# Kernel optimization log

Hardware: AMD Instinct MI355X
Metric: run time of the kernel (lower is better)

## Reference

```python
import jax, jax.numpy as jnp
import numpy as np

D_DIM = 128
K_DIM = 32


def setup_inputs() -> dict:
    key = jax.random.key(0)
    k1, k2, k3 = jax.random.split(key, 3)
    B, H, W = 8, 64, 64
    std1 = 1.0 / (K_DIM * D_DIM) ** 0.5
    std2 = 1.0 / K_DIM ** 0.5
    X = jax.random.normal(k1, (B, D_DIM, H, W), dtype=jnp.float32)
    codewords = jax.random.uniform(k2, (K_DIM, D_DIM), dtype=jnp.float32, minval=-std1, maxval=std1)
    scale = jax.random.uniform(k3, (K_DIM,), dtype=jnp.float32, minval=-std2, maxval=std2)
    return {"X": X, "codewords": codewords, "scale": scale}


def reference(X, codewords, scale):
    # X: [B, D, H, W] -> descriptors [B, N, D]
    B, D, H, W = X.shape
    Xf = X.reshape(B, D, H * W).transpose(0, 2, 1)  # [B, N, D]
    # Squared distance ||x - c||^2 expanded: avoids materializing [B,N,K,D]
    x_sq = jnp.sum(Xf * Xf, axis=-1, keepdims=True)          # [B, N, 1]
    c_sq = jnp.sum(codewords * codewords, axis=-1)           # [K]
    cross = jnp.einsum('bnd,kd->bnk', Xf, codewords)         # [B, N, K]
    dist2 = x_sq - 2.0 * cross + c_sq                        # [B, N, K]
    # NOTE: faithful to source -- softmax over scale * dist^2 (no negation)
    A = jax.nn.softmax(dist2 * scale, axis=-1)               # [B, N, K]
    # E[b,k,d] = sum_n A[b,n,k] * (x[b,n,d] - c[k,d])
    E = jnp.einsum('bnk,bnd->bkd', A, Xf) - jnp.sum(A, axis=1)[..., None] * codewords
    return E  # [B, K, D]
```

## Files before the change

kernel.cpp:

```cpp
#include <hip/hip_runtime.h>
#include <hip/hip_bf16.h>

#define D_DIM 128
#define K_DIM 32
#define NPIX  4096
#define TPB   128

typedef __bf16 bf16x8 __attribute__((ext_vector_type(8)));
typedef unsigned short u16x8 __attribute__((ext_vector_type(8)));
typedef float f32x4 __attribute__((ext_vector_type(4)));

__device__ __forceinline__ unsigned short f2bf(float f) {
    union { float f; unsigned u; } v; v.f = f;
    unsigned r = v.u + 0x7FFFu + ((v.u >> 16) & 1u);
    return (unsigned short)(r >> 16);
}
__device__ __forceinline__ unsigned pack2(float lo, float hi) {
    __hip_bfloat162 h = __float22bfloat162_rn(make_float2(lo, hi));
    union { __hip_bfloat162 b; unsigned u; } u; u.b = h;
    return u.u;
}
__device__ __forceinline__ float bf2f(unsigned short u) {
    union { unsigned u; float f; } v; v.u = ((unsigned)u) << 16;
    return v.f;
}
__device__ __forceinline__ bf16x8 ldfrag(const unsigned short* p) {
    union { u16x8 s; bf16x8 b; } u;
    u.s = *(const u16x8*)p;
    return u.b;
}
__device__ __forceinline__ bf16x8 pack8(float4 a, float4 b) {
    union { unsigned d[4]; bf16x8 v; } u;
    u.d[0] = pack2(a.x, a.y); u.d[1] = pack2(a.z, a.w);
    u.d[2] = pack2(b.x, b.y); u.d[3] = pack2(b.z, b.w);
    return u.v;
}

#define XND_LD 136
#define CW_LD  136
#define SA_LD  136

__global__ __launch_bounds__(256, 2) void enc_kernel(
    const float* __restrict__ X,
    const float* __restrict__ cw,
    const float* __restrict__ scale,
    float* __restrict__ out)
{
    __shared__ __align__(16) unsigned short sXnd[TPB * XND_LD];
    __shared__ __align__(16) unsigned short sCW[K_DIM * CW_LD];
    __shared__ __align__(16) unsigned short sA[K_DIM * SA_LD];
    __shared__ float sXsqP[8 * 129];
    __shared__ float sXsq[TPB];
    __shared__ float sSum[K_DIM];
    __shared__ float sSc[K_DIM];
    __shared__ float sCS[K_DIM];

    const int ltid = threadIdx.x;
    const int b    = blockIdx.x >> 5;
    const int n0   = (blockIdx.x & 31) * TPB;
    const int lane = ltid & 63;
    const int w    = ltid >> 6;
    const int l15  = lane & 15;
    const int quad = lane >> 4;

    if (ltid < K_DIM) {
        const float4* cr = (const float4*)(cw + ltid * D_DIM);
        float cs = 0.f;
        #pragma unroll 8
        for (int q = 0; q < 32; ++q) {
            float4 c4 = cr[q];
            cs = fmaf(c4.x, c4.x, fmaf(c4.y, c4.y, fmaf(c4.z, c4.z, fmaf(c4.w, c4.w, cs))));
        }
        float s = scale[ltid];
        sSc[ltid] = s;
        sCS[ltid] = cs * s;
        sSum[ltid] = 0.f;
    }

    {
        const int r  = ltid >> 3;
        const int q8 = ltid & 7;
        const float* cr = cw + r * D_DIM + 16 * q8;
        float4 c0 = *(const float4*)(cr + 0);
        float4 c1 = *(const float4*)(cr + 4);
        float4 c2 = *(const float4*)(cr + 8);
        float4 c3 = *(const float4*)(cr + 12);
        uint4 p0, p1;
        p0.x = pack2(c0.x, c0.y); p0.y = pack2(c0.z, c0.w);
        p0.z = pack2(c1.x, c1.y); p0.w = pack2(c1.z, c1.w);
        p1.x = pack2(c2.x, c2.y); p1.y = pack2(c2.z, c2.w);
        p1.z = pack2(c3.x, c3.y); p1.w = pack2(c3.z, c3.w);
        *(uint4*)&sCW[r * CW_LD + 16 * q8 + 0] = p0;
        *(uint4*)&sCW[r * CW_LD + 16 * q8 + 8] = p1;
    }

    {
        const int c = ltid & 31;
        const int r = ltid >> 5;
        float px[4] = {0.f, 0.f, 0.f, 0.f};
        const float* xb = X + (size_t)b * D_DIM * NPIX + n0;
        #pragma unroll
        for (int p = 0; p < 8; ++p) {
            const int d0 = 2 * (r + 8 * p);
            float4 f0 = *(const float4*)(xb + (size_t)d0 * NPIX + 4 * c);
            float4 f1 = *(const float4*)(xb + (size_t)(d0 + 1) * NPIX + 4 * c);
            px[0] = fmaf(f0.x, f0.x, fmaf(f1.x, f1.x, px[0]));
            px[1] = fmaf(f0.y, f0.y, fmaf(f1.y, f1.y, px[1]));
            px[2] = fmaf(f0.z, f0.z, fmaf(f1.z, f1.z, px[2]));
            px[3] = fmaf(f0.w, f0.w, fmaf(f1.w, f1.w, px[3]));
            *(unsigned*)&sXnd[(4 * c + 0) * XND_LD + d0] = pack2(f0.x, f1.x);
            *(unsigned*)&sXnd[(4 * c + 1) * XND_LD + d0] = pack2(f0.y, f1.y);
            *(unsigned*)&sXnd[(4 * c + 2) * XND_LD + d0] = pack2(f0.z, f1.z);
            *(unsigned*)&sXnd[(4 * c + 3) * XND_LD + d0] = pack2(f0.w, f1.w);
        }
        #pragma unroll
        for (int j = 0; j < 4; ++j) sXsqP[r * 129 + 4 * c + j] = px[j];
    }
    __syncthreads();

    if (ltid < TPB) {
        float s = 0.f;
        #pragma unroll
        for (int r = 0; r < 8; ++r) s += sXsqP[r * 129 + ltid];
        sXsq[ltid] = s;
    }

    f32x4 accA[2][2] = {{{0.f,0.f,0.f,0.f},{0.f,0.f,0.f,0.f}},
                        {{0.f,0.f,0.f,0.f},{0.f,0.f,0.f,0.f}}};
    {
        const int prow0 = (32 * w + l15) * XND_LD;
        const int prow1 = (32 * w + 16 + l15) * XND_LD;
        #pragma unroll
        for (int ks = 0; ks < 4; ++ks) {
            const int off = 8 * quad + 32 * ks;
            bf16x8 a0 = ldfrag(&sCW[l15 * CW_LD + off]);
            bf16x8 a1 = ldfrag(&sCW[(l15 + 16) * CW_LD + off]);
            bf16x8 b0 = ldfrag(&sXnd[prow0 + off]);
            bf16x8 b1 = ldfrag(&sXnd[prow1 + off]);
            accA[0][0] = __builtin_amdgcn_mfma_f32_16x16x32_bf16(a0, b0, accA[0][0], 0, 0, 0);
            accA[0][1] = __builtin_amdgcn_mfma_f32_16x16x32_bf16(a1, b0, accA[0][1], 0, 0, 0);
            accA[1][0] = __builtin_amdgcn_mfma_f32_16x16x32_bf16(a0, b1, accA[1][0], 0, 0, 0);
            accA[1][1] = __builtin_amdgcn_mfma_f32_16x16x32_bf16(a1, b1, accA[1][1], 0, 0, 0);
        }
    }
    __syncthreads();

    {
        float r8[8] = {0.f,0.f,0.f,0.f,0.f,0.f,0.f,0.f};
        #pragma unroll
        for (int pt = 0; pt < 2; ++pt) {
            const float xsq = sXsq[32 * w + 16 * pt + l15];
            float e8[8];
            float psum = 0.f;
            #pragma unroll
            for (int mt = 0; mt < 2; ++mt)
                #pragma unroll
                for (int reg = 0; reg < 4; ++reg) {
                    const int k = 16 * mt + 4 * quad + reg;
                    float l = fmaf(sSc[k], fmaf(-2.f, accA[pt][mt][reg], xsq), sCS[k]);
                    float e = __expf(l);
                    e8[4 * mt + reg] = e;
                    psum += e;
                }
            psum += __shfl_xor(psum, 16);
            psum += __shfl_xor(psum, 32);
            const float inv = 1.f / psum;
            #pragma unroll
            for (int i = 0; i < 8; ++i) {
                e8[i] *= inv;
                r8[i] += e8[i];
            }
            #pragma unroll
            for (int mt = 0; mt < 2; ++mt)
                #pragma unroll
                for (int reg = 0; reg < 4; ++reg) {
                    const int k = 16 * mt + 4 * quad + reg;
                    sA[k * SA_LD + 32 * w + 16 * pt + l15] = f2bf(e8[4 * mt + reg]);
                }
        }
        #pragma unroll
        for (int i = 0; i < 8; ++i) {
            r8[i] += __shfl_xor(r8[i], 1);
            r8[i] += __shfl_xor(r8[i], 2);
            r8[i] += __shfl_xor(r8[i], 4);
            r8[i] += __shfl_xor(r8[i], 8);
        }
        if (l15 == 0) {
            #pragma unroll
            for (int mt = 0; mt < 2; ++mt)
                #pragma unroll
                for (int reg = 0; reg < 4; ++reg)
                    atomicAdd(&sSum[16 * mt + 4 * quad + reg], r8[4 * mt + reg]);
        }
    }
    __syncthreads();

    f32x4 accE[2][2] = {{{0.f,0.f,0.f,0.f},{0.f,0.f,0.f,0.f}},
                        {{0.f,0.f,0.f,0.f},{0.f,0.f,0.f,0.f}}};
    #pragma unroll
    for (int dt = 0; dt < 2; ++dt) {
        const int d = 16 * (2 * w + dt) + l15;
        const float* xrow = X + ((size_t)b * D_DIM + d) * NPIX + n0;
        float4 g[4][2];
        #pragma unroll
        for (int ks = 0; ks < 4; ++ks) {
            const float* p = xrow + 8 * quad + 32 * ks;
            g[ks][0] = *(const float4*)p;
            g[ks][1] = *(const float4*)(p + 4);
        }
        #pragma unroll
        for (int ks = 0; ks < 4; ++ks) {
            const int off = 8 * quad + 32 * ks;
            bf16x8 bfrag = pack8(g[ks][0], g[ks][1]);
            bf16x8 a0 = ldfrag(&sA[l15 * SA_LD + off]);
            bf16x8 a1 = ldfrag(&sA[(l15 + 16) * SA_LD + off]);
            accE[dt][0] = __builtin_amdgcn_mfma_f32_16x16x32_bf16(a0, bfrag, accE[dt][0], 0, 0, 0);
            accE[dt][1] = __builtin_amdgcn_mfma_f32_16x16x32_bf16(a1, bfrag, accE[dt][1], 0, 0, 0);
        }
    }

    {
        float* outb = out + (size_t)b * (K_DIM * D_DIM);
        #pragma unroll
        for (int dt = 0; dt < 2; ++dt) {
            const int d = 16 * (2 * w + dt) + l15;
            #pragma unroll
            for (int mt = 0; mt < 2; ++mt) {
                #pragma unroll
                for (int rr = 0; rr < 4; ++rr) {
                    const int reg = (rr + blockIdx.x) & 3;
                    const int k = 16 * mt + 4 * quad + reg;
                    float sk  = sSum[k];
                    float cwv = bf2f(sCW[k * CW_LD + d]);
                    float v = fmaf(-sk, cwv, accE[dt][mt][reg]);
                    atomicAdd(outb + k * D_DIM + d, v);
                }
            }
        }
    }
}

extern "C" void kernel_launch(void* const* d_in, const int* in_sizes, int n_in,
                              void* d_out, int out_size, void* d_ws, size_t ws_size,
                              hipStream_t stream) {
    const float* X  = (const float*)d_in[0];
    const float* cw = (const float*)d_in[1];
    const float* sc = (const float*)d_in[2];
    float* out = (float*)d_out;
    (void)in_sizes; (void)n_in; (void)d_ws; (void)ws_size; (void)out_size;

    hipLaunchKernelGGL(enc_kernel, dim3(256), dim3(256), 0, stream, X, cw, sc, out);
}
```

Before: 71.82 us.

## Swizzle X tile in LDS with 16-byte stores and drop xsq reduction barrier

Restructures the X staging so each thread loads 8 consecutive channels and writes one packed 16-byte chunk per pixel into an XOR-swizzled LDS layout, replacing many 4-byte scattered stores. The MFMA B-fragment reads apply the matching swizzle. It also removes the separate x-squared reduction pass and its __syncthreads: each lane now sums the partial norms itself right before the softmax. The goal is fewer LDS bank conflicts and store instructions plus one less barrier, at the cost of some redundant LDS reads for the norm sums and more live registers.

```diff
diff --git a/kernel.cpp b/kernel.cpp
--- a/kernel.cpp
+++ b/kernel.cpp
@@ -50,7 +50,6 @@
     __shared__ __align__(16) unsigned short sCW[K_DIM * CW_LD];
     __shared__ __align__(16) unsigned short sA[K_DIM * SA_LD];
     __shared__ float sXsqP[8 * 129];
-    __shared__ float sXsq[TPB];
     __shared__ float sSum[K_DIM];
     __shared__ float sSc[K_DIM];
     __shared__ float sCS[K_DIM];
@@ -100,56 +99,73 @@
         float px[4] = {0.f, 0.f, 0.f, 0.f};
         const float* xb = X + (size_t)b * D_DIM * NPIX + n0;
         #pragma unroll
-        for (int p = 0; p < 8; ++p) {
-            const int d0 = 2 * (r + 8 * p);
-            float4 f0 = *(const float4*)(xb + (size_t)d0 * NPIX + 4 * c);
-            float4 f1 = *(const float4*)(xb + (size_t)(d0 + 1) * NPIX + 4 * c);
-            px[0] = fmaf(f0.x, f0.x, fmaf(f1.x, f1.x, px[0]));
-            px[1] = fmaf(f0.y, f0.y, fmaf(f1.y, f1.y, px[1]));
-            px[2] = fmaf(f0.z, f0.z, fmaf(f1.z, f1.z, px[2]));
-            px[3] = fmaf(f0.w, f0.w, fmaf(f1.w, f1.w, px[3]));
-            *(unsigned*)&sXnd[(4 * c + 0) * XND_LD + d0] = pack2(f0.x, f1.x);
-            *(unsigned*)&sXnd[(4 * c + 1) * XND_LD + d0] = pack2(f0.y, f1.y);
-            *(unsigned*)&sXnd[(4 * c + 2) * XND_LD + d0] = pack2(f0.z, f1.z);
-            *(unsigned*)&sXnd[(4 * c + 3) * XND_LD + d0] = pack2(f0.w, f1.w);
+        for (int h = 0; h < 2; ++h) {
+            float fx[8], fy[8], fz[8], fw[8];
+            #pragma unroll
+            for (int dd = 0; dd < 8; ++dd) {
+                const int d = 64 * h + 8 * r + dd;
+                float4 f = *(const float4*)(xb + (size_t)d * NPIX + 4 * c);
+                fx[dd] = f.x; fy[dd] = f.y; fz[dd] = f.z; fw[dd] = f.w;
+                px[0] = fmaf(f.x, f.x, px[0]);
+                px[1] = fmaf(f.y, f.y, px[1]);
+                px[2] = fmaf(f.z, f.z, px[2]);
+                px[3] = fmaf(f.w, f.w, px[3]);
+            }
+            const int pchunk = (r ^ (c & 7)) + 8 * h;
+            uint4 pk;
+            pk.x = pack2(fx[0], fx[1]); pk.y = pack2(fx[2], fx[3]);
+            pk.z = pack2(fx[4], fx[5]); pk.w = pack2(fx[6], fx[7]);
+            *(uint4*)&sXnd[(4 * c + 0) * XND_LD + 8 * pchunk] = pk;
+            pk.x = pack2(fy[0], fy[1]); pk.y = pack2(fy[2], fy[3]);
+            pk.z = pack2(fy[4], fy[5]); pk.w = pack2(fy[6], fy[7]);
+            *(uint4*)&sXnd[(4 * c + 1) * XND_LD + 8 * pchunk] = pk;
+            pk.x = pack2(fz[0], fz[1]); pk.y = pack2(fz[2], fz[3]);
+            pk.z = pack2(fz[4], fz[5]); pk.w = pack2(fz[6], fz[7]);
+            *(uint4*)&sXnd[(4 * c + 2) * XND_LD + 8 * pchunk] = pk;
+            pk.x = pack2(fw[0], fw[1]); pk.y = pack2(fw[2], fw[3]);
+            pk.z = pack2(fw[4], fw[5]); pk.w = pack2(fw[6], fw[7]);
+            *(uint4*)&sXnd[(4 * c + 3) * XND_LD + 8 * pchunk] = pk;
         }
         #pragma unroll
         for (int j = 0; j < 4; ++j) sXsqP[r * 129 + 4 * c + j] = px[j];
     }
     __syncthreads();
-
-    if (ltid < TPB) {
-        float s = 0.f;
-        #pragma unroll
-        for (int r = 0; r < 8; ++r) s += sXsqP[r * 129 + ltid];
-        sXsq[ltid] = s;
-    }
 
     f32x4 accA[2][2] = {{{0.f,0.f,0.f,0.f},{0.f,0.f,0.f,0.f}},
                         {{0.f,0.f,0.f,0.f},{0.f,0.f,0.f,0.f}}};
     {
         const int prow0 = (32 * w + l15) * XND_LD;
         const int prow1 = (32 * w + 16 + l15) * XND_LD;
+        const int xr0 = (l15 >> 2) & 7;
+        const int xr1 = ((l15 >> 2) + 4) & 7;
         #pragma unroll
         for (int ks = 0; ks < 4; ++ks) {
+            const int lg  = quad + 4 * ks;
+            const int ph0 = ((lg & 7) ^ xr0) + (lg & 8);
+            const int ph1 = ((lg & 7) ^ xr1) + (lg & 8);
             const int off = 8 * quad + 32 * ks;
             bf16x8 a0 = ldfrag(&sCW[l15 * CW_LD + off]);
             bf16x8 a1 = ldfrag(&sCW[(l15 + 16) * CW_LD + off]);
-            bf16x8 b0 = ldfrag(&sXnd[prow0 + off]);
-            bf16x8 b1 = ldfrag(&sXnd[prow1 + off]);
+            bf16x8 b0 = ldfrag(&sXnd[prow0 + 8 * ph0]);
+            bf16x8 b1 = ldfrag(&sXnd[prow1 + 8 * ph1]);
             accA[0][0] = __builtin_amdgcn_mfma_f32_16x16x32_bf16(a0, b0, accA[0][0], 0, 0, 0);
             accA[0][1] = __builtin_amdgcn_mfma_f32_16x16x32_bf16(a1, b0, accA[0][1], 0, 0, 0);
             accA[1][0] = __builtin_amdgcn_mfma_f32_16x16x32_bf16(a0, b1, accA[1][0], 0, 0, 0);
             accA[1][1] = __builtin_amdgcn_mfma_f32_16x16x32_bf16(a1, b1, accA[1][1], 0, 0, 0);
         }
     }
-    __syncthreads();
-
-    {
+
+    {
+        float xsq01[2] = {0.f, 0.f};
+        #pragma unroll
+        for (int r = 0; r < 8; ++r) {
+            xsq01[0] += sXsqP[r * 129 + 32 * w + l15];
+            xsq01[1] += sXsqP[r * 129 + 32 * w + 16 + l15];
+        }
         float r8[8] = {0.f,0.f,0.f,0.f,0.f,0.f,0.f,0.f};
         #pragma unroll
         for (int pt = 0; pt < 2; ++pt) {
-            const float xsq = sXsq[32 * w + 16 * pt + l15];
+            const float xsq = xsq01[pt];
             float e8[8];
             float psum = 0.f;
             #pragma unroll
```

Result: no change. 72.15 us (+0.5%).
